# Kernel optimization log

Measured on AMD Instinct MI355X. Metric: run time of the kernel, lower is better.

## Reference

```python
import jax, jax.numpy as jnp
import numpy as np

NU, NS, E, M = 200_000, 50_000, 1_000_000, 100_000
FU, FS, H = 64, 64, 128
UIN = 32 + 32 + FU  # user input dim after embedding concat = 128


def setup_inputs() -> dict:
    key = jax.random.key(0)
    ks = jax.random.split(key, 28)
    d = {}
    d["x_user_feat"] = jax.random.normal(ks[0], (NU, FU), jnp.float32)
    d["x_seller_feat"] = jax.random.normal(ks[1], (NS, FS), jnp.float32)
    d["x1"] = jax.random.randint(ks[2], (NU, 2), 0, 3, jnp.int32)  # col0 age<9, col1 gender<3
    d["src_user"] = jax.random.randint(ks[3], (E,), 0, NU, jnp.int32)
    d["dst_seller"] = jax.random.randint(ks[4], (E,), 0, NS, jnp.int32)
    d["src_seller"] = jax.random.randint(ks[5], (E,), 0, NS, jnp.int32)
    d["dst_user"] = jax.random.randint(ks[6], (E,), 0, NU, jnp.int32)
    d["mask_user"] = jax.random.randint(ks[7], (M,), 0, NU, jnp.int32)
    d["mask_seller"] = jax.random.randint(ks[8], (M,), 0, NS, jnp.int32)
    # embeddings
    d["age_emb"] = jax.random.normal(ks[9], (9, 32), jnp.float32)
    d["gen_emb"] = jax.random.normal(ks[10], (3, 32), jnp.float32)
    def w(k, i, o):
        return jax.random.normal(k, (i, o), jnp.float32) / np.sqrt(i).astype(np.float32)
    # layer 1: user update (neighbors are sellers), seller update (neighbors are users)
    d["W1ul"] = w(ks[11], FS, H); d["W1ur"] = w(ks[12], UIN, H); d["b1u"] = jnp.zeros((H,), jnp.float32)
    d["W1sl"] = w(ks[13], UIN, H); d["W1sr"] = w(ks[14], FS, H); d["b1s"] = jnp.zeros((H,), jnp.float32)
    # layer 2
    d["W2ul"] = w(ks[15], H, H); d["W2ur"] = w(ks[16], H, H); d["b2u"] = jnp.zeros((H,), jnp.float32)
    d["W2sl"] = w(ks[17], H, H); d["W2sr"] = w(ks[18], H, H); d["b2s"] = jnp.zeros((H,), jnp.float32)
    d["lin_w"] = w(ks[19], 2 * H, 1); d["lin_b"] = jnp.zeros((1,), jnp.float32)
    return d


def _sage(x_src, x_dst, src, dst, n_dst, Wl, Wr, b):
    # SAGEConv (mean aggr): lin_l(mean_{j in N(i)} x_src[j]) + lin_r(x_dst[i]) + b
    agg = jax.ops.segment_sum(x_src[src], dst, num_segments=n_dst)  # [n_dst, F_src]
    cnt = jax.ops.segment_sum(jnp.ones_like(dst, jnp.float32), dst, num_segments=n_dst)
    mean = agg / jnp.maximum(cnt, 1.0)[:, None]
    return mean @ Wl + x_dst @ Wr + b


def reference(x_user_feat, x_seller_feat, age_emb, gen_emb,
              W1ul, W1ur, b1u, W1sl, W1sr, b1s,
              W2ul, W2ur, b2u, W2sl, W2sr, b2s,
              lin_w, lin_b,
              x1, src_user, dst_seller, src_seller, dst_user,
              mask_user, mask_seller):
    # embedding concat for users
    x_u = jnp.concatenate([age_emb[x1[:, 0]], gen_emb[x1[:, 1]], x_user_feat], axis=1)  # [NU, 128]
    x_s = x_seller_feat  # [NS, 64]
    # layer 1 (HeteroConv aggr='sum' is trivial: one edge type per dst)
    u1 = _sage(x_s, x_u, src_seller, dst_user, NU, W1ul, W1ur, b1u)
    s1 = _sage(x_u, x_s, src_user, dst_seller, NS, W1sl, W1sr, b1s)
    u1, s1 = jax.nn.relu(u1), jax.nn.relu(s1)  # dropout p=0 -> identity
    # layer 2
    u2 = _sage(s1, u1, src_seller, dst_user, NU, W2ul, W2ur, b2u)
    s2 = _sage(u1, s1, src_user, dst_seller, NS, W2sl, W2sr, b2s)
    u2, s2 = jax.nn.relu(u2), jax.nn.relu(s2)
    # mask gather + final linear + sigmoid
    x = jnp.concatenate([u2[mask_user], s2[mask_seller]], axis=1)  # [M, 2H]
    return jax.nn.sigmoid(x @ lin_w + lin_b).reshape(-1)
```

## Files before the change

kernel.cpp:

```cpp
#include <hip/hip_runtime.h>
#include <math.h>

#define NU_N 200000
#define NS_N 50000
#define E_N  1000000
#define M_N  100000
#define NBU 782
#define NBS 196
#define NUBG 782
#define NSBG 196
#define EB 3907

typedef __attribute__((ext_vector_type(8))) short short8;
typedef __attribute__((ext_vector_type(16))) float f32x16;
typedef unsigned short ushort_t;
typedef unsigned int uint_t;

static constexpr size_t OFF_AGGU  = 0;
static constexpr size_t OFF_AGGS  = 51200000;
static constexpr size_t OFF_U     = 64000000;
static constexpr size_t OFF_S     = 115200256;
static constexpr size_t OFF_XU16  = 128000512;
static constexpr size_t OFF_XS16  = 153600640;
static constexpr size_t OFF_TBL27 = 160000768;
static constexpr size_t OFF_Z1U   = 160014592;
static constexpr size_t OFF_Z1S   = 160047360;
static constexpr size_t OFF_Z2U   = 160084224;
static constexpr size_t OFF_Z2S   = 160149760;
static constexpr size_t OFF_RPU   = 160215296;
static constexpr size_t OFF_RPS   = 161015312;
static constexpr size_t OFF_CSRU  = 161215328;
static constexpr size_t OFF_CSRS  = 165215360;
static constexpr size_t OFF_HIST  = 169215392;
static constexpr size_t OFF_PART  = 173615392;

__device__ inline ushort_t f2bf(float f) {
  union { float f; uint_t u; } c; c.f = f;
  uint_t r = (c.u + 0x7FFFu + ((c.u >> 16) & 1u)) >> 16;
  return (ushort_t)r;
}
__device__ inline float u2f(uint_t u) {
  union { uint_t u; float f; } c; c.u = u;
  return c.f;
}
__device__ inline float bf2f(uint_t u) { return u2f(u << 16); }

__global__ void histrank_k(const int* __restrict__ du, const int* __restrict__ ds,
                           int* __restrict__ histU, int* __restrict__ histS,
                           int* __restrict__ rU, int* __restrict__ rS) {
  int e = blockIdx.x * 256 + threadIdx.x;
  if (e >= E_N) return;
  rU[e] = atomicAdd(&histU[du[e]], 1);
  rS[e] = atomicAdd(&histS[ds[e]], 1);
}

__global__ void scan1_k(const int* __restrict__ histU, const int* __restrict__ histS,
                        int* __restrict__ rpU, int* __restrict__ rpS,
                        int* __restrict__ part) {
  __shared__ int s[256];
  int blk = blockIdx.x;
  const int* hist; int n; int* rowptr; int* pp;
  if (blk < NBU) { hist = histU; n = NU_N + 1; rowptr = rpU; pp = part; }
  else { blk -= NBU; hist = histS; n = NS_N + 1; rowptr = rpS; pp = part + 1024; }
  int t = threadIdx.x;
  int idx = blk * 256 + t;
  int v = (idx > 0 && idx < n) ? hist[idx - 1] : 0;
  s[t] = v;
  __syncthreads();
  for (int off = 1; off < 256; off <<= 1) {
    int x = (t >= off) ? s[t - off] : 0;
    __syncthreads();
    s[t] += x;
    __syncthreads();
  }
  if (idx < n) rowptr[idx] = s[t];
  if (t == 255) pp[blk] = s[255];
}

__global__ void scan2_k(int* __restrict__ part) {
  __shared__ int s[1024];
  int* pp = part + blockIdx.x * 1024;
  int nb = (blockIdx.x == 0) ? NBU : NBS;
  int t = threadIdx.x;
  int v = (t < nb) ? pp[t] : 0;
  s[t] = v;
  __syncthreads();
  for (int off = 1; off < 1024; off <<= 1) {
    int x = (t >= off) ? s[t - off] : 0;
    __syncthreads();
    s[t] += x;
    __syncthreads();
  }
  if (t < nb) pp[t] = s[t] - v;
}

__global__ void scan3_k(int* __restrict__ rpU, int* __restrict__ rpS,
                        const int* __restrict__ part) {
  int blk = blockIdx.x;
  int* rowptr; int n; const int* pp;
  if (blk < NBU) { rowptr = rpU; n = NU_N + 1; pp = part; }
  else { blk -= NBU; rowptr = rpS; n = NS_N + 1; pp = part + 1024; }
  int idx = blk * 256 + threadIdx.x;
  if (idx < n) rowptr[idx] += pp[blk];
}

__global__ void fillcsr_k(const int* __restrict__ du, const int* __restrict__ ds,
                          const int* __restrict__ su, const int* __restrict__ ss,
                          const int* __restrict__ rU, const int* __restrict__ rS,
                          const int* __restrict__ rpU, const int* __restrict__ rpS,
                          int* __restrict__ csrU, int* __restrict__ csrS) {
  int e = blockIdx.x * 256 + threadIdx.x;
  if (e >= E_N) return;
  int u = du[e];
  csrU[rpU[u] + rU[e]] = ss[e];
  int s = ds[e];
  csrS[rpS[s] + rS[e]] = su[e];
}

__global__ void prep_all_k(const float* __restrict__ xu, const float* __restrict__ xs,
                           const int* __restrict__ x1, const float* __restrict__ age,
                           const float* __restrict__ gen,
                           const float* __restrict__ W1ul, const float* __restrict__ W1ur,
                           const float* __restrict__ W1sl, const float* __restrict__ W1sr,
                           const float* __restrict__ W2ul, const float* __restrict__ W2ur,
                           const float* __restrict__ W2sl, const float* __restrict__ W2sr,
                           ushort_t* __restrict__ xu16, ushort_t* __restrict__ xs16,
                           ushort_t* __restrict__ ub, ushort_t* __restrict__ sb,
                           ushort_t* __restrict__ oh12,
                           float* __restrict__ tbl27,
                           ushort_t* __restrict__ z1u, ushort_t* __restrict__ z1s,
                           ushort_t* __restrict__ z2u, ushort_t* __restrict__ z2s) {
  int t = blockIdx.x * 256 + threadIdx.x;
  if (t < 4000000) {
    const float* src = (t < 3200000) ? xu : xs;
    ushort_t* dst = (t < 3200000) ? xu16 : xs16;
    int i = (t < 3200000) ? t : t - 3200000;
    float4 v = ((const float4*)src)[i];
    uint2 o;
    o.x = (uint_t)f2bf(v.x) | ((uint_t)f2bf(v.y) << 16);
    o.y = (uint_t)f2bf(v.z) | ((uint_t)f2bf(v.w) << 16);
    ((uint2*)dst)[i] = o;
  } else if (t < 4000100) {
    int t3 = t - 4000000;
    uint2 z; z.x = 0u; z.y = 0u;
    if (t3 < 16)       ((uint2*)xu16)[NU_N * 16 + t3] = z;
    else if (t3 < 32)  ((uint2*)xs16)[NS_N * 16 + (t3 - 16)] = z;
    else if (t3 < 64)  ((uint2*)ub)[NU_N * 32 + (t3 - 32)] = z;
    else if (t3 < 96)  ((uint2*)sb)[NS_N * 32 + (t3 - 64)] = z;
    else               ((uint2*)oh12)[NU_N * 4 + (t3 - 96)] = z;
  } else if (t < 4003556) {
    int i = t - 4000100;
    int tt = i >> 7, j = i & 127;
    int a = tt / 3, g = tt % 3;
    float acc = 0.f;
    for (int k = 0; k < 32; ++k) acc += age[a * 32 + k] * W1ur[k * 128 + j];
    for (int k = 0; k < 32; ++k) acc += gen[g * 32 + k] * W1ur[(32 + k) * 128 + j];
    tbl27[i] = acc;
  } else if (t < 4019940) {
    int i = t - 4003556;
    int j = i & 7, lane = (i >> 3) & 63, rest = i >> 9;
    int kt = rest % 8, ct = rest / 8;
    int k = kt * 16 + ((lane >> 5) << 3) + j;
    int n = ct * 32 + (lane & 31);
    float v = (k < 64) ? W1ul[k * 128 + n] : W1ur[k * 128 + n];
    z1u[i] = f2bf(v);
  } else if (t < 4038372) {
    int i = t - 4019940;
    int j = i & 7, lane = (i >> 3) & 63, rest = i >> 9;
    int kt = rest % 9, ct = rest / 9;
    int k = kt * 16 + ((lane >> 5) << 3) + j;
    int n = ct * 32 + (lane & 31);
    float v;
    if (k < 64) v = W1sl[(64 + k) * 128 + n];
    else if (k < 73) {
      int a = k - 64; v = 0.f;
      for (int kk = 0; kk < 32; ++kk) v += age[a * 32 + kk] * W1sl[kk * 128 + n];
    } else if (k < 76) {
      int g = k - 73; v = 0.f;
      for (int kk = 0; kk < 32; ++kk) v += gen[g * 32 + kk] * W1sl[(32 + kk) * 128 + n];
    } else if (k < 80) v = 0.f;
    else v = W1sr[(k - 80) * 128 + n];
    z1s[i] = f2bf(v);
  } else if (t < 4103908) {
    int i = t - 4038372;
    const float *Wl, *Wr; ushort_t* dst;
    if (i < 32768) { Wl = W2ul; Wr = W2ur; dst = z2u; }
    else { Wl = W2sl; Wr = W2sr; dst = z2s; i -= 32768; }
    int j = i & 7, lane = (i >> 3) & 63, rest = i >> 9;
    int kt = rest % 16, ct = rest / 16;
    int k = kt * 16 + ((lane >> 5) << 3) + j;
    int n = ct * 32 + (lane & 31);
    float v = (k < 128) ? Wl[k * 128 + n] : Wr[(k - 128) * 128 + n];
    dst[i] = f2bf(v);
  } else if (t < 4303908) {
    int r = t - 4103908;
    int2 ag = ((const int2*)x1)[r];
    uint_t wds[8];
#pragma unroll
    for (int ww = 0; ww < 8; ++ww) {
      int d0 = 2 * ww, d1 = 2 * ww + 1;
      uint_t lo = ((d0 == ag.x) || (d0 == 9 + ag.y)) ? 0x3F80u : 0u;
      uint_t hi = ((d1 == ag.x) || (d1 == 9 + ag.y)) ? 0x3F80u : 0u;
      wds[ww] = lo | (hi << 16);
    }
    uint4* orow = (uint4*)(oh12 + (size_t)r * 16);
    uint4 o0; o0.x = wds[0]; o0.y = wds[1]; o0.z = wds[2]; o0.w = wds[3];
    uint4 o1; o1.x = wds[4]; o1.y = wds[5]; o1.z = wds[6]; o1.w = wds[7];
    orow[0] = o0;
    orow[1] = o1;
  }
}

#define ACC8(V)                                              \
  acc[0] += bf2f(V.x); acc[1] += u2f(V.x & 0xffff0000u);     \
  acc[2] += bf2f(V.y); acc[3] += u2f(V.y & 0xffff0000u);     \
  acc[4] += bf2f(V.z); acc[5] += u2f(V.z & 0xffff0000u);     \
  acc[6] += bf2f(V.w); acc[7] += u2f(V.w & 0xffff0000u);

template <int R, int R1, int S1STR, int S2STR>
__device__ __forceinline__ void gmeanG(int b, int e, const int* __restrict__ csr,
                                       int zrow, const uint4* __restrict__ src1,
                                       const uint4* __restrict__ src2,
                                       uint4* __restrict__ dst, int c) {
  int n = e - b;
  const uint4* sp; int sstr; int cc;
  if (c < R1) { sp = src1; sstr = S1STR; cc = c; }
  else if (c < R) { sp = src2; sstr = S2STR; cc = c - R1; }
  else { sp = src1; sstr = S1STR; cc = 0; }
  float acc[8];
#pragma unroll
  for (int k = 0; k < 8; ++k) acc[k] = 0.f;
  int j = (n > 0) ? csr[b] : zrow;
  uint4 v = sp[(size_t)j * sstr + cc];
  for (int it = 0; it < n; ++it) {
    int j2 = (it + 1 < n) ? csr[b + it + 1] : zrow;
    uint4 v2 = sp[(size_t)j2 * sstr + cc];
    ACC8(v);
    v = v2;
  }
  if (c < R) {
    float inv = 1.0f / fmaxf((float)n, 1.0f);
    uint4 o;
    o.x = (uint_t)f2bf(acc[0] * inv) | ((uint_t)f2bf(acc[1] * inv) << 16);
    o.y = (uint_t)f2bf(acc[2] * inv) | ((uint_t)f2bf(acc[3] * inv) << 16);
    o.z = (uint_t)f2bf(acc[4] * inv) | ((uint_t)f2bf(acc[5] * inv) << 16);
    o.w = (uint_t)f2bf(acc[6] * inv) | ((uint_t)f2bf(acc[7] * inv) << 16);
    dst[c] = o;
  }
}

__global__ void gather1_k(const int* __restrict__ rpU, const int* __restrict__ csrU,
                          const ushort_t* __restrict__ xs16,
                          const int* __restrict__ rpS, const int* __restrict__ csrS,
                          const ushort_t* __restrict__ xu16,
                          const ushort_t* __restrict__ oh12,
                          ushort_t* __restrict__ aggU, ushort_t* __restrict__ aggS) {
  int wid = (blockIdx.x * 256 + threadIdx.x) >> 6;
  int lane = threadIdx.x & 63;
  if (wid < 25000) {
    int g = lane >> 3, c = lane & 7;
    int u = wid * 8 + g;
    gmeanG<8, 8, 8, 8>(rpU[u], rpU[u + 1], csrU, NS_N, (const uint4*)xs16,
                       (const uint4*)xs16, (uint4*)(aggU + (size_t)u * 64), c);
  } else {
    int w2 = wid - 25000;
    int g = lane >> 4, c = lane & 15;
    int s = w2 * 4 + g;
    gmeanG<10, 8, 8, 2>(rpS[s], rpS[s + 1], csrS, NU_N, (const uint4*)xu16,
                        (const uint4*)oh12, (uint4*)(aggS + (size_t)s * 80), c);
  }
}

__global__ void gather2_k(const int* __restrict__ rpU, const int* __restrict__ csrU,
                          const ushort_t* __restrict__ s1,
                          const int* __restrict__ rpS, const int* __restrict__ csrS,
                          const ushort_t* __restrict__ u1,
                          ushort_t* __restrict__ aggU, ushort_t* __restrict__ aggS) {
  int wid = (blockIdx.x * 256 + threadIdx.x) >> 6;
  int lane = threadIdx.x & 63;
  int g = lane >> 4, c = lane & 15;
  if (wid < 50000) {
    int u = wid * 4 + g;
    gmeanG<16, 16, 16, 16>(rpU[u], rpU[u + 1], csrU, NS_N, (const uint4*)s1,
                           (const uint4*)s1, (uint4*)(aggU + (size_t)u * 128), c);
  } else {
    int w2 = wid - 50000;
    int s = w2 * 4 + g;
    gmeanG<16, 16, 16, 16>(rpS[s], rpS[s + 1], csrS, NU_N, (const uint4*)u1,
                           (const uint4*)u1, (uint4*)(aggS + (size_t)s * 128), c);
  }
}

template <int KM, int KS, int SSTR, bool TBL>
__device__ __forceinline__ void gemm_core(
    short* sW, int bid, int nrows, const ushort_t* __restrict__ agg,
    const ushort_t* self, const ushort_t* __restrict__ wswz,
    const float* __restrict__ bias, const float* __restrict__ tbl27,
    const int* __restrict__ x1, ushort_t* out) {
  constexpr int K = KM + KS;
  constexpr int NKT = K / 16;
  {
    const uint4* g4 = (const uint4*)wswz;
    uint4* s4 = (uint4*)sW;
    for (int i = threadIdx.x; i < K * 16; i += 256) s4[i] = g4[i];
  }
  __syncthreads();

  int wave = threadIdx.x >> 6, lane = threadIdx.x & 63;
  int r0 = bid * 256 + wave * 64;
  int qk = (lane >> 5) << 3;

  int ra = r0 + (lane & 31), rb = ra + 32;
  int rac = (ra < nrows) ? ra : 0, rbc = (rb < nrows) ? rb : 0;

  f32x16 acc[2][4];
#pragma unroll
  for (int rt = 0; rt < 2; ++rt)
#pragma unroll
    for (int ct = 0; ct < 4; ++ct) acc[rt][ct] = (f32x16)0.0f;

  const short8* sWv = (const short8*)sW;

#pragma unroll
  for (int kt = 0; kt < NKT; ++kt) {
    int k0 = kt * 16 + qk;
    short8 af, bf;
    if (kt * 16 < KM) {
      af = *((const short8*)(agg + (size_t)rac * KM + k0));
      bf = *((const short8*)(agg + (size_t)rbc * KM + k0));
    } else {
      af = *((const short8*)(self + (size_t)rac * SSTR + (k0 - KM)));
      bf = *((const short8*)(self + (size_t)rbc * SSTR + (k0 - KM)));
    }
#pragma unroll
    for (int ct = 0; ct < 4; ++ct) {
      short8 wf = sWv[(ct * NKT + kt) * 64 + lane];
      acc[0][ct] = __builtin_amdgcn_mfma_f32_32x32x16_bf16(af, wf, acc[0][ct], 0, 0, 0);
      acc[1][ct] = __builtin_amdgcn_mfma_f32_32x32x16_bf16(bf, wf, acc[1][ct], 0, 0, 0);
    }
  }

  int nloc = lane & 31;
  float bn[4];
#pragma unroll
  for (int ct = 0; ct < 4; ++ct) bn[ct] = bias[ct * 32 + nloc];
  int rowq = 4 * (lane >> 5);
#pragma unroll
  for (int rt = 0; rt < 2; ++rt) {
#pragma unroll
    for (int reg = 0; reg < 16; ++reg) {
      int row = r0 + rt * 32 + (reg & 3) + 8 * (reg >> 2) + rowq;
      if (row < nrows) {
        const float* tp = nullptr;
        if (TBL) {
          int a = x1[2 * row], g = x1[2 * row + 1];
          tp = tbl27 + (a * 3 + g) * 128 + nloc;
        }
#pragma unroll
        for (int ct = 0; ct < 4; ++ct) {
          float v = acc[rt][ct][reg] + bn[ct];
          if (TBL) v += tp[ct * 32];
          out[(size_t)row * 128 + ct * 32 + nloc] = f2bf(fmaxf(v, 0.0f));
        }
      }
    }
  }
}

__global__ __launch_bounds__(256, 2) void gemm1_k(
    const ushort_t* __restrict__ aggU, const ushort_t* __restrict__ aggS,
    const ushort_t* __restrict__ xu16, const ushort_t* __restrict__ xs16,
    const ushort_t* __restrict__ z1u, const ushort_t* __restrict__ z1s,
    const float* __restrict__ b1u, const float* __restrict__ b1s,
    const float* __restrict__ tbl27, const int* __restrict__ x1,
    ushort_t* __restrict__ ub, ushort_t* __restrict__ sb) {
  extern __shared__ short smem[];
  if (blockIdx.x < NUBG)
    gemm_core<64, 64, 64, true>(smem, blockIdx.x, NU_N, aggU, xu16, z1u, b1u, tbl27, x1, ub);
  else
    gemm_core<80, 64, 64, false>(smem, blockIdx.x - NUBG, NS_N, aggS, xs16, z1s, b1s,
                                 nullptr, nullptr, sb);
}

__global__ __launch_bounds__(256, 2) void gemm2_k(
    const ushort_t* __restrict__ aggU, const ushort_t* __restrict__ aggS,
    const ushort_t* __restrict__ z2u, const ushort_t* __restrict__ z2s,
    const float* __restrict__ b2u, const float* __restrict__ b2s,
    ushort_t* ub, ushort_t* sb) {
  extern __shared__ short smem[];
  if (blockIdx.x < NUBG)
    gemm_core<128, 128, 128, false>(smem, blockIdx.x, NU_N, aggU, ub, z2u, b2u,
                                    nullptr, nullptr, ub);
  else
    gemm_core<128, 128, 128, false>(smem, blockIdx.x - NUBG, NS_N, aggS, sb, z2s, b2s,
                                    nullptr, nullptr, sb);
}

__global__ void final_k(const ushort_t* __restrict__ u2, const ushort_t* __restrict__ s2,
                        const int* __restrict__ mu, const int* __restrict__ ms,
                        const float* __restrict__ lw, const float* __restrict__ lb,
                        float* __restrict__ out) {
  int w = (blockIdx.x * blockDim.x + threadIdx.x) >> 6;
  int lane = threadIdx.x & 63;
  if (w >= M_N) return;
  int iu = mu[w], is = ms[w];
  uint_t a = ((const uint_t*)(u2 + (size_t)iu * 128))[lane];
  uint_t b = ((const uint_t*)(s2 + (size_t)is * 128))[lane];
  float p = bf2f(a & 0xffffu) * lw[2 * lane] + bf2f(a >> 16) * lw[2 * lane + 1]
          + bf2f(b & 0xffffu) * lw[128 + 2 * lane] + bf2f(b >> 16) * lw[129 + 2 * lane];
#pragma unroll
  for (int off = 32; off > 0; off >>= 1) p += __shfl_down(p, off, 64);
  if (lane == 0) out[w] = 1.0f / (1.0f + expf(-(p + lb[0])));
}

extern "C" void kernel_launch(void* const* d_in, const int* in_sizes, int n_in,
                              void* d_out, int out_size, void* d_ws, size_t ws_size,
                              hipStream_t stream) {
  const float* xu   = (const float*)d_in[0];
  const float* xs   = (const float*)d_in[1];
  const int*   x1   = (const int*)d_in[2];
  const int*   su   = (const int*)d_in[3];
  const int*   ds   = (const int*)d_in[4];
  const int*   ss   = (const int*)d_in[5];
  const int*   du   = (const int*)d_in[6];
  const int*   mu   = (const int*)d_in[7];
  const int*   ms   = (const int*)d_in[8];
  const float* age  = (const float*)d_in[9];
  const float* gen  = (const float*)d_in[10];
  const float* W1ul = (const float*)d_in[11];
  const float* W1ur = (const float*)d_in[12];
  const float* b1u  = (const float*)d_in[13];
  const float* W1sl = (const float*)d_in[14];
  const float* W1sr = (const float*)d_in[15];
  const float* b1s  = (const float*)d_in[16];
  const float* W2ul = (const float*)d_in[17];
  const float* W2ur = (const float*)d_in[18];
  const float* b2u  = (const float*)d_in[19];
  const float* W2sl = (const float*)d_in[20];
  const float* W2sr = (const float*)d_in[21];
  const float* b2s  = (const float*)d_in[22];
  const float* lw   = (const float*)d_in[23];
  const float* lb   = (const float*)d_in[24];

  char* w = (char*)d_ws;
  ushort_t* aggU = (ushort_t*)(w + OFF_AGGU);
  ushort_t* aggS = (ushort_t*)(w + OFF_AGGS);
  ushort_t* ub   = (ushort_t*)(w + OFF_U);
  ushort_t* sb   = (ushort_t*)(w + OFF_S);
  ushort_t* xu16 = (ushort_t*)(w + OFF_XU16);
  ushort_t* xs16 = (ushort_t*)(w + OFF_XS16);
  float* tbl27   = (float*)(w + OFF_TBL27);
  ushort_t* z1u  = (ushort_t*)(w + OFF_Z1U);
  ushort_t* z1s  = (ushort_t*)(w + OFF_Z1S);
  ushort_t* z2u  = (ushort_t*)(w + OFF_Z2U);
  ushort_t* z2s  = (ushort_t*)(w + OFF_Z2S);
  int* rpU    = (int*)(w + OFF_RPU);
  int* rpS    = (int*)(w + OFF_RPS);
  int* csrU   = (int*)(w + OFF_CSRU);
  int* csrS   = (int*)(w + OFF_CSRS);
  int* histU  = (int*)(w + OFF_HIST);
  int* histS  = (int*)(w + OFF_HIST + 800000);
  int* rankU  = (int*)(w + OFF_AGGU);
  int* rankS  = (int*)(w + OFF_AGGU + 4000000);
  ushort_t* oh12 = (ushort_t*)(w + OFF_U);
  int* part   = (int*)(w + OFF_PART);
  float* out = (float*)d_out;

  hipMemsetAsync(w + OFF_HIST, 0, 1000000, stream);
  histrank_k<<<EB, 256, 0, stream>>>(du, ds, histU, histS, rankU, rankS);
  scan1_k<<<NBU + NBS, 256, 0, stream>>>(histU, histS, rpU, rpS, part);
  scan2_k<<<2, 1024, 0, stream>>>(part);
  scan3_k<<<NBU + NBS, 256, 0, stream>>>(rpU, rpS, part);
  fillcsr_k<<<EB, 256, 0, stream>>>(du, ds, su, ss, rankU, rankS, rpU, rpS, csrU, csrS);
  prep_all_k<<<16813, 256, 0, stream>>>(xu, xs, x1, age, gen,
                                        W1ul, W1ur, W1sl, W1sr, W2ul, W2ur, W2sl, W2sr,
                                        xu16, xs16, ub, sb, oh12, tbl27,
                                        z1u, z1s, z2u, z2s);

  gather1_k<<<9375, 256, 0, stream>>>(rpU, csrU, xs16, rpS, csrS, xu16, oh12,
                                      aggU, aggS);
  gemm1_k<<<NUBG + NSBG, 256, 144 * 128 * 2, stream>>>(aggU, aggS, xu16, xs16, z1u, z1s,
                                                       b1u, b1s, tbl27, x1, ub, sb);

  gather2_k<<<15625, 256, 0, stream>>>(rpU, csrU, sb, rpS, csrS, ub, aggU, aggS);
  gemm2_k<<<NUBG + NSBG, 256, 256 * 128 * 2, stream>>>(aggU, aggS, z2u, z2s,
                                                       b2u, b2s, ub, sb);

  final_k<<<(M_N * 64 + 255) / 256, 256, 0, stream>>>(ub, sb, mu, ms, lw, lb, out);
}
```

Before: 536.1 us.

## Build CSR via two-level bucketed counting sort with LDS histograms

Replaces the global-atomic histogram, rank and random-scatter CSR build with a two-pass bucketed counting sort. Edges are first histogrammed into coarse node buckets per edge chunk using shared-memory atomics, then the chunk-by-bucket count matrix is scanned and edges are scattered as (node, value) pairs into bucket-contiguous temporaries. A per-bucket kernel then builds row pointers and the final CSR locally in LDS. This is meant to cut global atomic contention and scattered writes, at the cost of extra kernels and an intermediate pass through memory.

```diff
diff --git a/kernel.cpp b/kernel.cpp
--- a/kernel.cpp
+++ b/kernel.cpp
@@ -5,11 +5,14 @@
 #define NS_N 50000
 #define E_N  1000000
 #define M_N  100000
-#define NBU 782
-#define NBS 196
 #define NUBG 782
 #define NSBG 196
-#define EB 3907
+
+#define CH_E 2048
+#define NCH  489
+#define NBKT 391
+#define CM   191199
+#define NCB  747
 
 typedef __attribute__((ext_vector_type(8))) short short8;
 typedef __attribute__((ext_vector_type(16))) float f32x16;
@@ -31,8 +34,14 @@
 static constexpr size_t OFF_RPS   = 161015312;
 static constexpr size_t OFF_CSRU  = 161215328;
 static constexpr size_t OFF_CSRS  = 165215360;
-static constexpr size_t OFF_HIST  = 169215392;
 static constexpr size_t OFF_PART  = 173615392;
+
+static constexpr size_t OFF_TMPU = OFF_AGGU;
+static constexpr size_t OFF_TMPS = OFF_AGGU + 8000000;
+static constexpr size_t OFF_CMU  = OFF_AGGS;
+static constexpr size_t OFF_CMS  = OFF_AGGS + 764800;
+static constexpr size_t OFF_CMUS = OFF_AGGS + 1529600;
+static constexpr size_t OFF_CMSS = OFF_AGGS + 2294400;
 
 __device__ inline ushort_t f2bf(float f) {
   union { float f; uint_t u; } c; c.f = f;
@@ -45,26 +54,34 @@
 }
 __device__ inline float bf2f(uint_t u) { return u2f(u << 16); }
 
-__global__ void histrank_k(const int* __restrict__ du, const int* __restrict__ ds,
-                           int* __restrict__ histU, int* __restrict__ histS,
-                           int* __restrict__ rU, int* __restrict__ rS) {
-  int e = blockIdx.x * 256 + threadIdx.x;
-  if (e >= E_N) return;
-  rU[e] = atomicAdd(&histU[du[e]], 1);
-  rS[e] = atomicAdd(&histS[ds[e]], 1);
-}
-
-__global__ void scan1_k(const int* __restrict__ histU, const int* __restrict__ histS,
-                        int* __restrict__ rpU, int* __restrict__ rpS,
+__global__ void hist_lds_k(const int* __restrict__ du, const int* __restrict__ ds,
+                           int* __restrict__ cmatU, int* __restrict__ cmatS) {
+  __shared__ int h[NBKT];
+  int side = blockIdx.x >= NCH;
+  int c = side ? blockIdx.x - NCH : blockIdx.x;
+  const int* nd = side ? ds : du;
+  int shift = side ? 7 : 9;
+  int* cm = side ? cmatS : cmatU;
+  for (int i = threadIdx.x; i < NBKT; i += 256) h[i] = 0;
+  __syncthreads();
+  int e0 = c * CH_E, e1 = min(E_N, e0 + CH_E);
+  for (int e = e0 + (int)threadIdx.x; e < e1; e += 256)
+    atomicAdd(&h[nd[e] >> shift], 1);
+  __syncthreads();
+  for (int b = threadIdx.x; b < NBKT; b += 256) cm[b * NCH + c] = h[b];
+}
+
+__global__ void scan1_k(const int* __restrict__ cmU, const int* __restrict__ cmS,
+                        int* __restrict__ outU, int* __restrict__ outS,
                         int* __restrict__ part) {
   __shared__ int s[256];
   int blk = blockIdx.x;
-  const int* hist; int n; int* rowptr; int* pp;
-  if (blk < NBU) { hist = histU; n = NU_N + 1; rowptr = rpU; pp = part; }
-  else { blk -= NBU; hist = histS; n = NS_N + 1; rowptr = rpS; pp = part + 1024; }
+  const int* in; int* out; int* pp;
+  if (blk < NCB) { in = cmU; out = outU; pp = part; }
+  else { blk -= NCB; in = cmS; out = outS; pp = part + 1024; }
   int t = threadIdx.x;
   int idx = blk * 256 + t;
-  int v = (idx > 0 && idx < n) ? hist[idx - 1] : 0;
+  int v = (idx > 0 && idx <= CM) ? in[idx - 1] : 0;
   s[t] = v;
   __syncthreads();
   for (int off = 1; off < 256; off <<= 1) {
@@ -73,14 +90,14 @@
     s[t] += x;
     __syncthreads();
   }
-  if (idx < n) rowptr[idx] = s[t];
+  if (idx < CM) out[idx] = s[t];
   if (t == 255) pp[blk] = s[255];
 }
 
 __global__ void scan2_k(int* __restrict__ part) {
   __shared__ int s[1024];
   int* pp = part + blockIdx.x * 1024;
-  int nb = (blockIdx.x == 0) ? NBU : NBS;
+  int nb = NCB;
   int t = threadIdx.x;
   int v = (t < nb) ? pp[t] : 0;
   s[t] = v;
@@ -94,27 +111,87 @@
   if (t < nb) pp[t] = s[t] - v;
 }
 
-__global__ void scan3_k(int* __restrict__ rpU, int* __restrict__ rpS,
+__global__ void scan3_k(int* __restrict__ outU, int* __restrict__ outS,
                         const int* __restrict__ part) {
   int blk = blockIdx.x;
-  int* rowptr; int n; const int* pp;
-  if (blk < NBU) { rowptr = rpU; n = NU_N + 1; pp = part; }
-  else { blk -= NBU; rowptr = rpS; n = NS_N + 1; pp = part + 1024; }
+  int* out; const int* pp;
+  if (blk < NCB) { out = outU; pp = part; }
+  else { blk -= NCB; out = outS; pp = part + 1024; }
   int idx = blk * 256 + threadIdx.x;
-  if (idx < n) rowptr[idx] += pp[blk];
-}
-
-__global__ void fillcsr_k(const int* __restrict__ du, const int* __restrict__ ds,
+  if (idx < CM) out[idx] += pp[blk];
+}
+
+__global__ void scatter_k(const int* __restrict__ du, const int* __restrict__ ds,
                           const int* __restrict__ su, const int* __restrict__ ss,
-                          const int* __restrict__ rU, const int* __restrict__ rS,
-                          const int* __restrict__ rpU, const int* __restrict__ rpS,
-                          int* __restrict__ csrU, int* __restrict__ csrS) {
-  int e = blockIdx.x * 256 + threadIdx.x;
-  if (e >= E_N) return;
-  int u = du[e];
-  csrU[rpU[u] + rU[e]] = ss[e];
-  int s = ds[e];
-  csrS[rpS[s] + rS[e]] = su[e];
+                          const int* __restrict__ cmUs, const int* __restrict__ cmSs,
+                          int2* __restrict__ tmpU, int2* __restrict__ tmpS) {
+  __shared__ int cur[NBKT];
+  int side = blockIdx.x >= NCH;
+  int c = side ? blockIdx.x - NCH : blockIdx.x;
+  const int* nd = side ? ds : du;
+  const int* vv = side ? su : ss;
+  const int* cms = side ? cmSs : cmUs;
+  int2* tmp = side ? tmpS : tmpU;
+  int shift = side ? 7 : 9;
+  for (int b = threadIdx.x; b < NBKT; b += 256) cur[b] = cms[b * NCH + c];
+  __syncthreads();
+  int e0 = c * CH_E, e1 = min(E_N, e0 + CH_E);
+  for (int e = e0 + (int)threadIdx.x; e < e1; e += 256) {
+    int node = nd[e];
+    int pos = atomicAdd(&cur[node >> shift], 1);
+    int2 p; p.x = node; p.y = vv[e];
+    tmp[pos] = p;
+  }
+}
+
+__global__ void build_k(const int* __restrict__ cmUs, const int* __restrict__ cmSs,
+                        const int2* __restrict__ tmpU, const int2* __restrict__ tmpS,
+                        int* __restrict__ rpU, int* __restrict__ rpS,
+                        int* __restrict__ csrU, int* __restrict__ csrS) {
+  __shared__ int cnt[512];
+  __shared__ int s2[256];
+  __shared__ int base[512];
+  int side = blockIdx.x >= NBKT;
+  int b = side ? blockIdx.x - NBKT : blockIdx.x;
+  const int* cms = side ? cmSs : cmUs;
+  const int2* tmp = side ? tmpS : tmpU;
+  int* rp = side ? rpS : rpU;
+  int* csr = side ? csrS : csrU;
+  int nper = side ? 128 : 512;
+  int nn = side ? NS_N : NU_N;
+  int t = threadIdx.x;
+  int start = cms[b * NCH];
+  int end = (b + 1 < NBKT) ? cms[(b + 1) * NCH] : E_N;
+  cnt[t] = 0; cnt[t + 256] = 0;
+  __syncthreads();
+  int nbase = b * nper;
+  for (int i = start + t; i < end; i += 256) atomicAdd(&cnt[tmp[i].x - nbase], 1);
+  __syncthreads();
+  int a0 = cnt[2 * t], a1 = cnt[2 * t + 1];
+  s2[t] = a0 + a1;
+  __syncthreads();
+  int v = s2[t];
+  for (int off = 1; off < 256; off <<= 1) {
+    int x = (t >= off) ? s2[t - off] : 0;
+    __syncthreads();
+    s2[t] += x;
+    __syncthreads();
+  }
+  int ex = s2[t] - v;
+  base[2 * t] = start + ex;
+  base[2 * t + 1] = start + ex + a0;
+  __syncthreads();
+  for (int i = t; i < nper; i += 256) {
+    int node = nbase + i;
+    if (node < nn) rp[node] = base[i];
+  }
+  if (b == NBKT - 1 && t == 0) rp[nn] = E_N;
+  __syncthreads();
+  for (int i = start + t; i < end; i += 256) {
+    int2 p = tmp[i];
+    int pos = atomicAdd(&base[p.x - nbase], 1);
+    csr[pos] = p.y;
+  }
 }
 
 __global__ void prep_all_k(const float* __restrict__ xu, const float* __restrict__ xs,
@@ -458,20 +535,23 @@
   int* rpS    = (int*)(w + OFF_RPS);
   int* csrU   = (int*)(w + OFF_CSRU);
   int* csrS   = (int*)(w + OFF_CSRS);
-  int* histU  = (int*)(w + OFF_HIST);
-  int* histS  = (int*)(w + OFF_HIST + 800000);
-  int* rankU  = (int*)(w + OFF_AGGU);
-  int* rankS  = (int*)(w + OFF_AGGU + 4000000);
+  int2* tmpU  = (int2*)(w + OFF_TMPU);
+  int2* tmpS  = (int2*)(w + OFF_TMPS);
+  int* cmatU  = (int*)(w + OFF_CMU);
+  int* cmatS  = (int*)(w + OFF_CMS);
+  int* cmatUs = (int*)(w + OFF_CMUS);
+  int* cmatSs = (int*)(w + OFF_CMSS);
   ushort_t* oh12 = (ushort_t*)(w + OFF_U);
   int* part   = (int*)(w + OFF_PART);
   float* out = (float*)d_out;
 
-  hipMemsetAsync(w + OFF_HIST, 0, 1000000, stream);
-  histrank_k<<<EB, 256, 0, stream>>>(du, ds, histU, histS, rankU, rankS);
-  scan1_k<<<NBU + NBS, 256, 0, stream>>>(histU, histS, rpU, rpS, part);
+  hist_lds_k<<<2 * NCH, 256, 0, stream>>>(du, ds, cmatU, cmatS);
+  scan1_k<<<2 * NCB, 256, 0, stream>>>(cmatU, cmatS, cmatUs, cmatSs, part);
   scan2_k<<<2, 1024, 0, stream>>>(part);
-  scan3_k<<<NBU + NBS, 256, 0, stream>>>(rpU, rpS, part);
-  fillcsr_k<<<EB, 256, 0, stream>>>(du, ds, su, ss, rankU, rankS, rpU, rpS, csrU, csrS);
+  scan3_k<<<2 * NCB, 256, 0, stream>>>(cmatUs, cmatSs, part);
+  scatter_k<<<2 * NCH, 256, 0, stream>>>(du, ds, su, ss, cmatUs, cmatSs, tmpU, tmpS);
+  build_k<<<2 * NBKT, 256, 0, stream>>>(cmatUs, cmatSs, tmpU, tmpS,
+                                        rpU, rpS, csrU, csrS);
   prep_all_k<<<16813, 256, 0, stream>>>(xu, xs, x1, age, gen,
                                         W1ul, W1ur, W1sl, W1sr, W2ul, W2ur, W2sl, W2sr,
                                         xu16, xs16, ub, sb, oh12, tbl27,
```

Result: faster. 458.7 us (-14.4%).
